# Performance work log

Measured on AMD Instinct MI355X. Metric: run time of the kernel, lower is better.

The kernel has to match this reference:

```python
import jax, jax.numpy as jnp
import numpy as np

B, T, E, H = 8, 1024, 512, 8  # batch, seq, emb (= per-head dim!), heads


def _layernorm(x, g, b, eps=1e-5):
    mu = jnp.mean(x, axis=-1, keepdims=True)
    var = jnp.var(x, axis=-1, keepdims=True)
    return (x - mu) * jax.lax.rsqrt(var + eps) * g + b


def setup_inputs() -> dict:
    key = jax.random.key(0)
    ks = jax.random.split(key, 8)
    s_in = 1.0 / np.sqrt(E)
    s_he = 1.0 / np.sqrt(H * E)
    return {
        "x": jax.random.normal(ks[0], (B, T, E), jnp.float32),
        "Wq": jax.random.normal(ks[1], (E, H * E), jnp.float32) * s_in,
        "bq": jnp.zeros((H * E,), jnp.float32),
        "Wk": jax.random.normal(ks[2], (E, H * E), jnp.float32) * s_in,
        "bk": jnp.zeros((H * E,), jnp.float32),
        "Wv": jax.random.normal(ks[3], (E, H * E), jnp.float32) * s_in,
        "bv": jnp.zeros((H * E,), jnp.float32),
        "Wu": jax.random.normal(ks[4], (H * E, E), jnp.float32) * s_he,
        "bu": jnp.zeros((E,), jnp.float32),
        "g1": jnp.ones((E,), jnp.float32),
        "b1": jnp.zeros((E,), jnp.float32),
        "Wh": jax.random.normal(ks[5], (E, E), jnp.float32) * s_in,
        "bh": jnp.zeros((E,), jnp.float32),
        "g2": jnp.ones((E,), jnp.float32),
        "b2": jnp.zeros((E,), jnp.float32),
    }


def reference(x, Wq, bq, Wk, bk, Wv, bv, Wu, bu, g1, b1, Wh, bh, g2, b2):
    b, t, e = x.shape
    h = Wq.shape[1] // e
    norm = 1.0 / np.sqrt(e)
    # projections: (b,t,h,e); each head gets full emb width per the source
    q = (x @ Wq + bq).reshape(b, t, h, e) * norm
    k = (x @ Wk + bk).reshape(b, t, h, e) * norm
    v = (x @ Wv + bv).reshape(b, t, h, e)
    # scores (b,h,t,t); Q and K are BOTH scaled (norm_factor applied to each)
    dot = jnp.einsum("bqhe,bkhe->bhqk", q, k)
    attn = jax.nn.softmax(dot, axis=-1)
    out = jnp.einsum("bhqk,bkhe->bqhe", attn, v)  # (b,t,h,e)
    out = out.reshape(b, t, h * e).sum(axis=1)     # sum over time -> (b,h*e)
    out = jax.nn.relu(out @ Wu + bu)               # unifyheads + active_func, (b,e)
    # dropout p=0 -> identity
    x = _layernorm(x + out[:, None, :], g1, b1)
    x = _layernorm(x + jax.nn.relu(x @ Wh + bh), g2, b2)
    return x
```

## Files before the change

kernel.cpp:

```cpp
#include <hip/hip_runtime.h>

#define BB 8
#define TT 1024
#define EE 512
#define HH 8
#define HEE 4096

typedef unsigned short u16;
typedef unsigned char u8;
typedef __bf16 bf16x8 __attribute__((ext_vector_type(8)));
typedef float floatx4 __attribute__((ext_vector_type(4)));
typedef float floatx2 __attribute__((ext_vector_type(2)));

__device__ __forceinline__ u16 f2bf(float f) {
    union { float f; unsigned int i; } v; v.f = f;
    unsigned int x = v.i;
    x += 0x7fffu + ((x >> 16) & 1u);
    return (u16)(x >> 16);
}
__device__ __forceinline__ float bf2f(u16 u) {
    union { unsigned int i; float f; } v; v.i = ((unsigned int)u) << 16; return v.f;
}
__device__ __forceinline__ void glds16(const u16* g, u16* l) {
    __builtin_amdgcn_global_load_lds(
        (const __attribute__((address_space(1))) void*)g,
        (__attribute__((address_space(3))) void*)l, 16, 0, 0);
}

__global__ __launch_bounds__(256) void convx_kernel(
    const float* __restrict__ x, u16* __restrict__ xb)
{
    size_t i = ((size_t)blockIdx.x * 256 + threadIdx.x) * 8;
    float4 a = *(const float4*)&x[i];
    float4 b = *(const float4*)&x[i + 4];
    union { u16 s[8]; uint4 v; } t;
    t.s[0] = f2bf(a.x); t.s[1] = f2bf(a.y); t.s[2] = f2bf(a.z); t.s[3] = f2bf(a.w);
    t.s[4] = f2bf(b.x); t.s[5] = f2bf(b.y); t.s[6] = f2bf(b.z); t.s[7] = f2bf(b.w);
    *(uint4*)&xb[i] = t.v;
}

__global__ __launch_bounds__(256) void transpose_wh(
    const float* __restrict__ Wh, u16* __restrict__ Wht)
{
    int n0 = blockIdx.x << 6, k0 = blockIdx.y << 6;
    __shared__ u16 tile[64][72];
    int tid = threadIdx.x;
    for (int rep = 0; rep < 4; rep++) {
        int lin = tid + (rep << 8);
        int r = lin >> 4, c4 = (lin & 15) << 2;
        float4 v = *(const float4*)&Wh[(size_t)(k0 + r) * EE + n0 + c4];
        union { u16 s[4]; uint2 u; } t;
        t.s[0] = f2bf(v.x); t.s[1] = f2bf(v.y); t.s[2] = f2bf(v.z); t.s[3] = f2bf(v.w);
        *(uint2*)&tile[r][c4] = t.u;
    }
    __syncthreads();
    for (int rep = 0; rep < 2; rep++) {
        int lin = tid + (rep << 8);
        int rr = lin >> 3, cc8 = (lin & 7) << 3;
        union { u16 s[8]; uint4 v; } tmp;
        #pragma unroll
        for (int u2 = 0; u2 < 8; u2++) tmp.s[u2] = tile[cc8 + u2][rr];
        *(uint4*)&Wht[(size_t)(n0 + rr) * EE + k0 + cc8] = tmp.v;
    }
}

__global__ __launch_bounds__(256) void mh_kernel(
    const float* __restrict__ Wq, const float* __restrict__ Wk, u16* __restrict__ Mt)
{
    __shared__ u16 As[128][40];
    __shared__ u16 Bs[128][40];
    int et = blockIdx.x, ft = blockIdx.y, h = blockIdx.z;
    int tid = threadIdx.x;
    int f0 = ft << 7, e0 = et << 7, hb = h << 9;
    int w = tid >> 6, lane = tid & 63;
    int g = lane >> 4, mn = lane & 15;
    int wm = (w >> 1) << 6, wn = (w & 1) << 6;
    floatx4 acc[4][4];
    floatx4 zero = {0.f, 0.f, 0.f, 0.f};
    for (int i = 0; i < 4; i++) for (int j = 0; j < 4; j++) acc[i][j] = zero;

    for (int kk = 0; kk < EE; kk += 32) {
        __syncthreads();
        for (int rep = 0; rep < 2; rep++) {
            int lin = tid + (rep << 8);
            int row = lin >> 2, c8 = (lin & 3) << 3;
            float4 va = *(const float4*)&Wk[(size_t)(f0 + row) * HEE + hb + kk + c8];
            float4 vb = *(const float4*)&Wk[(size_t)(f0 + row) * HEE + hb + kk + c8 + 4];
            union { u16 s[8]; uint4 v; } ta;
            ta.s[0]=f2bf(va.x); ta.s[1]=f2bf(va.y); ta.s[2]=f2bf(va.z); ta.s[3]=f2bf(va.w);
            ta.s[4]=f2bf(vb.x); ta.s[5]=f2bf(vb.y); ta.s[6]=f2bf(vb.z); ta.s[7]=f2bf(vb.w);
            *(uint4*)&As[row][c8] = ta.v;
            float4 vc = *(const float4*)&Wq[(size_t)(e0 + row) * HEE + hb + kk + c8];
            float4 vd = *(const float4*)&Wq[(size_t)(e0 + row) * HEE + hb + kk + c8 + 4];
            union { u16 s[8]; uint4 v; } tb;
            tb.s[0]=f2bf(vc.x); tb.s[1]=f2bf(vc.y); tb.s[2]=f2bf(vc.z); tb.s[3]=f2bf(vc.w);
            tb.s[4]=f2bf(vd.x); tb.s[5]=f2bf(vd.y); tb.s[6]=f2bf(vd.z); tb.s[7]=f2bf(vd.w);
            *(uint4*)&Bs[row][c8] = tb.v;
        }
        __syncthreads();
        bf16x8 af[4], bfr[4];
        #pragma unroll
        for (int i = 0; i < 4; i++) af[i]  = *(const bf16x8*)&As[wm + (i << 4) + mn][g << 3];
        #pragma unroll
        for (int j = 0; j < 4; j++) bfr[j] = *(const bf16x8*)&Bs[wn + (j << 4) + mn][g << 3];
        #pragma unroll
        for (int i = 0; i < 4; i++)
            #pragma unroll
            for (int j = 0; j < 4; j++)
                acc[i][j] = __builtin_amdgcn_mfma_f32_16x16x32_bf16(af[i], bfr[j], acc[i][j], 0, 0, 0);
    }
    const float norm2 = 0.001953125f;
    #pragma unroll
    for (int i = 0; i < 4; i++)
        #pragma unroll
        for (int j = 0; j < 4; j++) {
            int e = e0 + wn + (j << 4) + mn;
            #pragma unroll
            for (int r = 0; r < 4; r++) {
                int f = f0 + wm + (i << 4) + (g << 2) + r;
                Mt[(size_t)(hb + f) * EE + e] = f2bf(acc[i][j][r] * norm2);
            }
        }
}

__global__ __launch_bounds__(256) void p_proj(
    const u16* __restrict__ xb, const u16* __restrict__ Mt, u16* __restrict__ P)
{
    int id = blockIdx.x;
    int xcd = id & 7, v = id >> 3;
    int mt = v >> 2, cg = v & 3;
    int nt = (cg << 3) + xcd;
    __shared__ u16 As[128][32];
    __shared__ u16 Bs[128][32];
    int tid = threadIdx.x;
    int n0 = nt << 7, m0 = mt << 7;
    int w = tid >> 6, lane = tid & 63;
    int g = lane >> 4, mn = lane & 15;
    int wm = (w >> 1) << 6, wn = (w & 1) << 6;
    floatx4 acc[4][4];
    floatx4 zero = {0.f, 0.f, 0.f, 0.f};
    for (int i = 0; i < 4; i++) for (int j = 0; j < 4; j++) acc[i][j] = zero;

    int srow = tid >> 2, sc8 = (tid & 3) << 3;
    const u16* ga = xb + (size_t)(m0 + srow) * EE + sc8;
    const u16* gb = Mt + (size_t)(n0 + srow) * EE + sc8;
    u16* la = &As[0][0] + tid * 8;
    u16* lb = &Bs[0][0] + tid * 8;

    #pragma unroll
    for (int kk = 0; kk < EE; kk += 32) {
        __syncthreads();
        glds16(ga + kk, la);
        glds16(ga + kk + (size_t)64 * EE, la + 2048);
        glds16(gb + kk, lb);
        glds16(gb + kk + (size_t)64 * EE, lb + 2048);
        __syncthreads();
        bf16x8 af[4], bfr[4];
        #pragma unroll
        for (int i = 0; i < 4; i++) af[i]  = *(const bf16x8*)&As[wm + (i << 4) + mn][g << 3];
        #pragma unroll
        for (int j = 0; j < 4; j++) bfr[j] = *(const bf16x8*)&Bs[wn + (j << 4) + mn][g << 3];
        #pragma unroll
        for (int i = 0; i < 4; i++)
            #pragma unroll
            for (int j = 0; j < 4; j++)
                acc[i][j] = __builtin_amdgcn_mfma_f32_16x16x32_bf16(af[i], bfr[j], acc[i][j], 0, 0, 0);
    }
    #pragma unroll
    for (int i = 0; i < 4; i++)
        #pragma unroll
        for (int j = 0; j < 4; j++) {
            int col = n0 + wn + (j << 4) + mn;
            int h = col >> 9, f = col & 511;
            #pragma unroll
            for (int r = 0; r < 4; r++) {
                int row = m0 + wm + (i << 4) + (g << 2) + r;
                int bl = row >> 10, t = row & 1023;
                P[(((size_t)bl * HH + h) * TT + t) * EE + f] = f2bf(acc[i][j][r]);
            }
        }
}

__global__ __launch_bounds__(512) void spass1_kernel(
    const u16* __restrict__ P, const u16* __restrict__ xbf,
    u8* __restrict__ U, float* __restrict__ lpart)
{
    __shared__ u16 As[3][8192];
    __shared__ u16 Bs[3][8192];
    int id = blockIdx.x;
    int xcd = id & 7, v = id >> 3;
    int sl = ((v >> 4) << 3) + xcd;
    int tile = v & 15;
    int kt = tile >> 2, qt = tile & 3;
    int tid = threadIdx.x;
    int w = tid >> 6, lane = tid & 63;
    int g = lane >> 4, mn = lane & 15;
    int wm = w >> 2, wn = w & 3;

    const u16* Abase = xbf + ((size_t)(sl >> 3) * TT + (kt << 8)) * EE;
    const u16* Bbase = P   + ((size_t)sl * TT + (qt << 8)) * EE;

    int srow = tid >> 2;
    int cs = (tid & 3) ^ ((tid >> 3) & 3);
    const u16* gA = Abase + (size_t)srow * EE + (cs << 3);
    const u16* gB = Bbase + (size_t)srow * EE + (cs << 3);
    u16* lA = &As[0][0] + tid * 8;
    u16* lB = &Bs[0][0] + tid * 8;

    int coff = (g ^ ((mn >> 1) & 3)) << 3;
    int raBase = ((wm << 7) + mn) << 5;
    int rbBase = ((wn << 6) + mn) << 5;

    floatx4 acc[8][4];
    floatx4 zero = {0.f, 0.f, 0.f, 0.f};
    #pragma unroll
    for (int i = 0; i < 8; i++)
        #pragma unroll
        for (int j = 0; j < 4; j++) acc[i][j] = zero;

    #define STG_A(t, b) do { \
        glds16(gA + ((t) << 5),                    lA + (b) * 8192); \
        glds16(gA + ((t) << 5) + (size_t)128 * EE, lA + (b) * 8192 + 4096); \
    } while (0)
    #define STG_B(t, b) do { \
        glds16(gB + ((t) << 5),                    lB + (b) * 8192); \
        glds16(gB + ((t) << 5) + (size_t)128 * EE, lB + (b) * 8192 + 4096); \
    } while (0)

    STG_A(0, 0); STG_B(0, 0);
    STG_A(1, 1); STG_B(1, 1);
    asm volatile("s_waitcnt vmcnt(4)" ::: "memory");
    __builtin_amdgcn_s_barrier();
    __builtin_amdgcn_sched_barrier(0);

    #pragma unroll
    for (int t = 0; t < 16; t++) {
        const int cur = t % 3;
        const int nxt = (t + 2) % 3;
        bf16x8 af0[4], bfr[4];
        #pragma unroll
        for (int i = 0; i < 4; i++)
            af0[i] = *(const bf16x8*)&As[cur][raBase + (i << 9) + coff];
        #pragma unroll
        for (int j = 0; j < 4; j++)
            bfr[j] = *(const bf16x8*)&Bs[cur][rbBase + (j << 9) + coff];
        if (t < 14) STG_A(t + 2, nxt);
        __builtin_amdgcn_sched_barrier(0);
        __builtin_amdgcn_s_barrier();
        asm volatile("s_waitcnt lgkmcnt(0)" ::: "memory");
        __builtin_amdgcn_sched_barrier(0);
        __builtin_amdgcn_s_setprio(1);
        #pragma unroll
        for (int i = 0; i < 4; i++)
            #pragma unroll
            for (int j = 0; j < 4; j++)
                acc[i][j] = __builtin_amdgcn_mfma_f32_16x16x32_bf16(af0[i], bfr[j], acc[i][j], 0, 0, 0);
        __builtin_amdgcn_s_setprio(0);
        __builtin_amdgcn_sched_barrier(0);
        __builtin_amdgcn_s_barrier();
        bf16x8 af1[4];
        #pragma unroll
        for (int i = 0; i < 4; i++)
            af1[i] = *(const bf16x8*)&As[cur][raBase + ((i + 4) << 9) + coff];
        if (t < 14) STG_B(t + 2, nxt);
        __builtin_amdgcn_sched_barrier(0);
        __builtin_amdgcn_s_barrier();
        asm volatile("s_waitcnt lgkmcnt(0)" ::: "memory");
        __builtin_amdgcn_sched_barrier(0);
        __builtin_amdgcn_s_setprio(1);
        #pragma unroll
        for (int i = 0; i < 4; i++)
            #pragma unroll
            for (int j = 0; j < 4; j++)
                acc[i + 4][j] = __builtin_amdgcn_mfma_f32_16x16x32_bf16(af1[i], bfr[j], acc[i + 4][j], 0, 0, 0);
        __builtin_amdgcn_s_setprio(0);
        __builtin_amdgcn_sched_barrier(0);
        if (t < 14)      asm volatile("s_waitcnt vmcnt(4)" ::: "memory");
        else if (t == 14) asm volatile("s_waitcnt vmcnt(0)" ::: "memory");
        __builtin_amdgcn_s_barrier();
        __builtin_amdgcn_sched_barrier(0);
    }
    #undef STG_A
    #undef STG_B

    float rsj[4] = {0.f, 0.f, 0.f, 0.f};
    u8* Ub = U + ((size_t)sl << 20) + (kt << 8) + (wm << 7) + (g << 2);
    #pragma unroll
    for (int j = 0; j < 4; j++) {
        int q = (qt << 8) + (wn << 6) + (j << 4) + mn;
        u8* Uq = Ub + ((size_t)q << 10);
        #pragma unroll
        for (int i = 0; i < 8; i++) {
            float e0 = __expf(acc[i][j][0]);
            float e1 = __expf(acc[i][j][1]);
            float e2 = __expf(acc[i][j][2]);
            float e3 = __expf(acc[i][j][3]);
            rsj[j] += (e0 + e1) + (e2 + e3);
            int pk = __builtin_amdgcn_cvt_pk_fp8_f32(e0, e1, 0, false);
            pk = __builtin_amdgcn_cvt_pk_fp8_f32(e2, e3, pk, true);
            *(unsigned int*)(Uq + (i << 4)) = (unsigned int)pk;
        }
    }
    #pragma unroll
    for (int j = 0; j < 4; j++) {
        rsj[j] += __shfl_xor(rsj[j], 16, 64);
        rsj[j] += __shfl_xor(rsj[j], 32, 64);
    }
    float* red = (float*)&As[0][0];
    if (g == 0) {
        #pragma unroll
        for (int j = 0; j < 4; j++)
            red[(wm << 8) + (wn << 6) + (j << 4) + mn] = rsj[j];
    }
    __syncthreads();
    if (tid < 256) {
        float s = red[tid] + red[256 + tid];
        lpart[(((size_t)(sl * 4 + kt)) << 10) + (qt << 8) + tid] = s;
    }
}

__global__ __launch_bounds__(256) void colreduce_kernel(
    const u8* __restrict__ U, const float* __restrict__ lpart,
    float* __restrict__ wpart)
{
    __shared__ float lin[128];
    int sl = blockIdx.x, qc = blockIdx.y;
    int tid = threadIdx.x;
    if (tid < 128) {
        float s = 0.f;
        #pragma unroll
        for (int kt = 0; kt < 4; kt++)
            s += lpart[((size_t)(sl * 4 + kt) << 10) + (qc << 7) + tid];
        lin[tid] = 1.f / s;
    }
    __syncthreads();
    const u8* Us = U + ((size_t)sl << 20) + ((size_t)(qc << 7) << 10) + (tid << 2);
    float a0 = 0.f, a1 = 0.f, a2 = 0.f, a3 = 0.f;
    #pragma unroll 8
    for (int q = 0; q < 128; q++) {
        unsigned int d = *(const unsigned int*)(Us + ((size_t)q << 10));
        float l = lin[q];
        floatx2 lo = __builtin_amdgcn_cvt_pk_f32_fp8((int)d, false);
        floatx2 hi = __builtin_amdgcn_cvt_pk_f32_fp8((int)d, true);
        a0 += l * lo[0];
        a1 += l * lo[1];
        a2 += l * hi[0];
        a3 += l * hi[1];
    }
    float4 res = {a0, a1, a2, a3};
    *(float4*)&wpart[(((size_t)sl * 8 + qc) << 10) + (tid << 2)] = res;
}

__global__ __launch_bounds__(256) void sv_kernel(
    const u16* __restrict__ xb, const float* __restrict__ wpart, float* __restrict__ sVp)
{
    __shared__ float wl[8][128];
    int b = blockIdx.x, kq = blockIdx.y;
    int tid = threadIdx.x;
    #pragma unroll
    for (int rep = 0; rep < 4; rep++) {
        int idx = tid + (rep << 8);
        int h = idx >> 7, k = idx & 127;
        float s = 0.f;
        #pragma unroll
        for (int qt = 0; qt < 8; qt++)
            s += wpart[(((size_t)(b * 8 + h)) * 8 + qt) * TT + (kq << 7) + k];
        wl[h][k] = s;
    }
    __syncthreads();
    const u16* xr = xb + ((size_t)b * TT + (kq << 7)) * EE;
    float a0[8], a1[8];
    #pragma unroll
    for (int h = 0; h < 8; h++) { a0[h] = 0.f; a1[h] = 0.f; }
    for (int k = 0; k < 128; k++) {
        float x0 = bf2f(xr[(size_t)k * EE + tid]);
        float x1 = bf2f(xr[(size_t)k * EE + tid + 256]);
        #pragma unroll
        for (int h = 0; h < 8; h++) {
            float wk = wl[h][k];
            a0[h] += wk * x0;
            a1[h] += wk * x1;
        }
    }
    #pragma unroll
    for (int h = 0; h < 8; h++) {
        sVp[((size_t)b * 8 + kq) * HEE + (h << 9) + tid]       = a0[h];
        sVp[((size_t)b * 8 + kq) * HEE + (h << 9) + tid + 256] = a1[h];
    }
}

__global__ __launch_bounds__(256) void out1_kernel(
    const float* __restrict__ sVp, const float* __restrict__ Wv,
    const float* __restrict__ bv, float* __restrict__ o1)
{
    __shared__ float s[8][512];
    __shared__ float part[4][8][64];
    int h = blockIdx.x, ec = blockIdx.y;
    int tid = threadIdx.x;
    for (int idx = tid; idx < 8 * 512; idx += 256) {
        int b = idx >> 9, e = idx & 511;
        float acc = 0.f;
        #pragma unroll
        for (int kq = 0; kq < 8; kq++)
            acc += sVp[((size_t)b * 8 + kq) * HEE + (h << 9) + e];
        s[b][e] = acc;
    }
    __syncthreads();
    int cl = tid & 63, eq = tid >> 6;
    int col = (h << 9) + (ec << 6) + cl;
    float a[8];
    #pragma unroll
    for (int b = 0; b < 8; b++) a[b] = 0.f;
    for (int e = eq << 7; e < (eq << 7) + 128; e++) {
        float wv = Wv[(size_t)e * HEE + col];
        #pragma unroll
        for (int b = 0; b < 8; b++) a[b] += s[b][e] * wv;
    }
    #pragma unroll
    for (int b = 0; b < 8; b++) part[eq][b][cl] = a[b];
    __syncthreads();
    #pragma unroll
    for (int r = 0; r < 2; r++) {
        int idx2 = tid + (r << 8);
        int b = idx2 >> 6, c2 = idx2 & 63;
        int col2 = (h << 9) + (ec << 6) + c2;
        float vv = part[0][b][c2] + part[1][b][c2] + part[2][b][c2] + part[3][b][c2]
                 + 1024.f * bv[col2];
        o1[(size_t)b * HEE + col2] = vv;
    }
}

__global__ __launch_bounds__(256) void out2_kernel(
    const float* __restrict__ o1, const float* __restrict__ Wu, float* __restrict__ o2p)
{
    __shared__ float o1s[8][128];
    __shared__ float part[4][8][64];
    int jc = blockIdx.x, ec = blockIdx.y;
    int tid = threadIdx.x;
    #pragma unroll
    for (int it = 0; it < 4; it++) {
        int idx = tid + (it << 8);
        int b = idx >> 7, jj = idx & 127;
        o1s[b][jj] = o1[(size_t)b * HEE + (jc << 7) + jj];
    }
    __syncthreads();
    int el = tid & 63, jq = tid >> 6;
    int col = (ec << 6) + el;
    const float* wu = Wu + (size_t)((jc << 7) + (jq << 5)) * EE + col;
    float a[8];
    #pragma unroll
    for (int b = 0; b < 8; b++) a[b] = 0.f;
    #pragma unroll 4
    for (int jj = 0; jj < 32; jj++) {
        float wv = wu[(size_t)jj * EE];
        int j = (jq << 5) + jj;
        #pragma unroll
        for (int b = 0; b < 8; b++) a[b] += o1s[b][j] * wv;
    }
    #pragma unroll
    for (int b = 0; b < 8; b++) part[jq][b][el] = a[b];
    __syncthreads();
    #pragma unroll
    for (int it = 0; it < 2; it++) {
        int idx = tid + (it << 8);
        int b = idx >> 6, e2 = idx & 63;
        float vv = part[0][b][e2] + part[1][b][e2] + part[2][b][e2] + part[3][b][e2];
        o2p[((size_t)b * 32 + jc) * EE + (ec << 6) + e2] = vv;
    }
}

__global__ __launch_bounds__(512) void out2_reduce(
    const float* __restrict__ o2p, const float* __restrict__ bu, float* __restrict__ o2)
{
    int b = blockIdx.x, tid = threadIdx.x;
    float s = bu[tid];
    for (int jc = 0; jc < 32; jc++)
        s += o2p[((size_t)b * 32 + jc) * EE + tid];
    o2[(size_t)b * EE + tid] = fmaxf(s, 0.f);
}

__global__ __launch_bounds__(256) void tail_fused(
    const float* __restrict__ x, const float* __restrict__ o2,
    const float* __restrict__ g1, const float* __restrict__ b1,
    const u16* __restrict__ Wht, const float* __restrict__ bh,
    const float* __restrict__ g2, const float* __restrict__ b2,
    float* __restrict__ out)
{
    __shared__ u16 Ys[32][520];
    __shared__ u16 Bs[512][32];
    __shared__ float redS[4][32];
    __shared__ float redQ[4][32];
    int tid = threadIdx.x;
    int m0 = blockIdx.x << 5;
    int b = m0 >> 10;
    int w = tid >> 6, lane = tid & 63;
    int g = lane >> 4, mn = lane & 15;

    {
        int c8 = lane << 3;
        float ob[8], g1v[8], b1v[8];
        ((float4*)ob)[0]  = *(const float4*)&o2[(size_t)b * EE + c8];
        ((float4*)ob)[1]  = *(const float4*)&o2[(size_t)b * EE + c8 + 4];
        ((float4*)g1v)[0] = *(const float4*)&g1[c8];
        ((float4*)g1v)[1] = *(const float4*)&g1[c8 + 4];
        ((float4*)b1v)[0] = *(const float4*)&b1[c8];
        ((float4*)b1v)[1] = *(const float4*)&b1[c8 + 4];
        for (int iter = 0; iter < 8; iter++) {
            int row = w + (iter << 2);
            const float* xr = x + (size_t)(m0 + row) * EE + c8;
            float v[8];
            ((float4*)v)[0] = *(const float4*)&xr[0];
            ((float4*)v)[1] = *(const float4*)&xr[4];
            float s = 0.f, q = 0.f;
            #pragma unroll
            for (int u2 = 0; u2 < 8; u2++) {
                v[u2] += ob[u2];
                s += v[u2];
                q += v[u2] * v[u2];
            }
            #pragma unroll
            for (int off = 1; off < 64; off <<= 1) {
                s += __shfl_xor(s, off, 64);
                q += __shfl_xor(q, off, 64);
            }
            float mean = s * (1.f / EE);
            float var = q * (1.f / EE) - mean * mean;
            float rstd = rsqrtf(var + 1e-5f);
            union { u16 us[8]; uint4 uv; } pk;
            #pragma unroll
            for (int u2 = 0; u2 < 8; u2++)
                pk.us[u2] = f2bf((v[u2] - mean) * rstd * g1v[u2] + b1v[u2]);
            *(uint4*)&Ys[row][c8] = pk.uv;
        }
    }

    int n0w = w << 7;
    floatx4 acc[2][8];
    floatx4 zero = {0.f, 0.f, 0.f, 0.f};
    for (int i = 0; i < 2; i++) for (int j = 0; j < 8; j++) acc[i][j] = zero;

    for (int kk = 0; kk < EE; kk += 32) {
        __syncthreads();
        #pragma unroll
        for (int c = 0; c < 8; c++) {
            int lin = (c << 8) + tid;
            int nrow = lin >> 2, k8 = (lin & 3) << 3;
            glds16(Wht + (size_t)nrow * EE + kk + k8, &Bs[0][0] + lin * 8);
        }
        __syncthreads();
        bf16x8 af[2], bfr[8];
        #pragma unroll
        for (int i = 0; i < 2; i++)
            af[i] = *(const bf16x8*)&Ys[(i << 4) + mn][kk + (g << 3)];
        #pragma unroll
        for (int j = 0; j < 8; j++)
            bfr[j] = *(const bf16x8*)&Bs[n0w + (j << 4) + mn][g << 3];
        #pragma unroll
        for (int i = 0; i < 2; i++)
            #pragma unroll
            for (int j = 0; j < 8; j++)
                acc[i][j] = __builtin_amdgcn_mfma_f32_16x16x32_bf16(af[i], bfr[j], acc[i][j], 0, 0, 0);
    }

    float bh8[8], g28[8], b28[8];
    #pragma unroll
    for (int j = 0; j < 8; j++) {
        int col = n0w + (j << 4) + mn;
        bh8[j] = bh[col]; g28[j] = g2[col]; b28[j] = b2[col];
    }
    float ps[2][4], pq[2][4];
    #pragma unroll
    for (int i = 0; i < 2; i++)
        #pragma unroll
        for (int r = 0; r < 4; r++) { ps[i][r] = 0.f; pq[i][r] = 0.f; }
    #pragma unroll
    for (int i = 0; i < 2; i++)
        #pragma unroll
        for (int j = 0; j < 8; j++) {
            int col = n0w + (j << 4) + mn;
            #pragma unroll
            for (int r = 0; r < 4; r++) {
                int row = (i << 4) + (g << 2) + r;
                float zv = fmaxf(acc[i][j][r] + bh8[j], 0.f) + bf2f(Ys[row][col]);
                acc[i][j][r] = zv;
                ps[i][r] += zv;
                pq[i][r] += zv * zv;
            }
        }
    #pragma unroll
    for (int off = 1; off < 16; off <<= 1) {
        #pragma unroll
        for (int i = 0; i < 2; i++)
            #pragma unroll
            for (int r = 0; r < 4; r++) {
                ps[i][r] += __shfl_xor(ps[i][r], off, 64);
                pq[i][r] += __shfl_xor(pq[i][r], off, 64);
            }
    }
    if (mn == 0) {
        #pragma unroll
        for (int i = 0; i < 2; i++)
            #pragma unroll
            for (int r = 0; r < 4; r++) {
                int row = (i << 4) + (g << 2) + r;
                redS[w][row] = ps[i][r];
                redQ[w][row] = pq[i][r];
            }
    }
    __syncthreads();
    #pragma unroll
    for (int i = 0; i < 2; i++)
        #pragma unroll
        for (int r = 0; r < 4; r++) {
            int row = (i << 4) + (g << 2) + r;
            float s = redS[0][row] + redS[1][row] + redS[2][row] + redS[3][row];
            float q = redQ[0][row] + redQ[1][row] + redQ[2][row] + redQ[3][row];
            float mean = s * (1.f / EE);
            float var = q * (1.f / EE) - mean * mean;
            float rstd = rsqrtf(var + 1e-5f);
            #pragma unroll
            for (int j = 0; j < 8; j++) {
                int col = n0w + (j << 4) + mn;
                out[(size_t)(m0 + row) * EE + col] =
                    (acc[i][j][r] - mean) * rstd * g28[j] + b28[j];
            }
        }
}

extern "C" void kernel_launch(void* const* d_in, const int* in_sizes, int n_in,
                              void* d_out, int out_size, void* d_ws, size_t ws_size,
                              hipStream_t stream)
{
    const float* x  = (const float*)d_in[0];
    const float* Wq = (const float*)d_in[1];
    const float* Wk = (const float*)d_in[3];
    const float* Wv = (const float*)d_in[5];
    const float* bv = (const float*)d_in[6];
    const float* Wu = (const float*)d_in[7];
    const float* bu = (const float*)d_in[8];
    const float* g1 = (const float*)d_in[9];
    const float* b1 = (const float*)d_in[10];
    const float* Wh = (const float*)d_in[11];
    const float* bh = (const float*)d_in[12];
    const float* g2 = (const float*)d_in[13];
    const float* b2 = (const float*)d_in[14];
    float* out = (float*)d_out;

    char* p = (char*)d_ws;
    u16* Wht = (u16*)p;    p += (size_t)EE * EE * 2;
    u16* xbf = (u16*)p;    p += (size_t)BB * TT * EE * 2;
    u16* Mt  = (u16*)p;    p += (size_t)HEE * EE * 2;
    float* lpart = (float*)p; p += (size_t)64 * 8 * TT * 4;
    float* wpart = (float*)p; p += (size_t)64 * 8 * TT * 4;
    float* sVp   = (float*)p; p += (size_t)BB * 8 * HEE * 4;
    float* o1    = (float*)p; p += (size_t)BB * HEE * 4;
    float* o2p   = (float*)p; p += (size_t)BB * 32 * EE * 4;
    float* o2    = (float*)p; p += (size_t)BB * EE * 4;
    u16* P  = (u16*)p;     p += (size_t)BB * HH * TT * EE * 2;
    u8* U   = (u8*)p;      p += (size_t)64 * TT * TT;

    convx_kernel<<<dim3(2048), 256, 0, stream>>>(x, xbf);
    transpose_wh<<<dim3(8, 8), 256, 0, stream>>>(Wh, Wht);
    mh_kernel<<<dim3(4, 4, 8), 256, 0, stream>>>(Wq, Wk, Mt);
    p_proj<<<dim3(2048), 256, 0, stream>>>(xbf, Mt, P);
    spass1_kernel<<<dim3(1024), 512, 0, stream>>>(P, xbf, U, lpart);
    colreduce_kernel<<<dim3(64, 8), 256, 0, stream>>>(U, lpart, wpart);
    sv_kernel<<<dim3(8, 8), 256, 0, stream>>>(xbf, wpart, sVp);
    out1_kernel<<<dim3(8, 8), 256, 0, stream>>>(sVp, Wv, bv, o1);
    out2_kernel<<<dim3(32, 8), 256, 0, stream>>>(o1, Wu, o2p);
    out2_reduce<<<dim3(8), 512, 0, stream>>>(o2p, bu, o2);
    tail_fused<<<dim3(256), 256, 0, stream>>>(x, o2, g1, b1, Wht, bh, g2, b2, out);
}
```

Before: 355.8 us.

## Fuse P projection into score kernel, merge prep kernels, atomic out2 reduction

The P = x·M projection is now computed per (batch, head, 128-query tile) inside the score kernel and kept in shared memory, so the large bf16 P tensor is never written to or read back from global memory. Inside the same block it then loops over four key tiles to compute exp scores, writes fp8 U through a shared-memory staging buffer, and emits the row-sum partials. The x conversion, the Wh transpose and the o2 bias init are merged into one launch. out2 now accumulates with atomicAdd into o2, with the ReLU moved into tail_fused, which removes the separate reduce kernel. In exchange the fused kernel uses large shared memory (160KB) and launches only 512 blocks, which limits occupancy. Float atomics also make the summation order nondeterministic.

```diff
diff --git a/kernel.cpp b/kernel.cpp
--- a/kernel.cpp
+++ b/kernel.cpp
@@ -27,40 +27,46 @@
         (__attribute__((address_space(3))) void*)l, 16, 0, 0);
 }
 
-__global__ __launch_bounds__(256) void convx_kernel(
-    const float* __restrict__ x, u16* __restrict__ xb)
-{
-    size_t i = ((size_t)blockIdx.x * 256 + threadIdx.x) * 8;
-    float4 a = *(const float4*)&x[i];
-    float4 b = *(const float4*)&x[i + 4];
-    union { u16 s[8]; uint4 v; } t;
-    t.s[0] = f2bf(a.x); t.s[1] = f2bf(a.y); t.s[2] = f2bf(a.z); t.s[3] = f2bf(a.w);
-    t.s[4] = f2bf(b.x); t.s[5] = f2bf(b.y); t.s[6] = f2bf(b.z); t.s[7] = f2bf(b.w);
-    *(uint4*)&xb[i] = t.v;
-}
-
-__global__ __launch_bounds__(256) void transpose_wh(
-    const float* __restrict__ Wh, u16* __restrict__ Wht)
-{
-    int n0 = blockIdx.x << 6, k0 = blockIdx.y << 6;
+__global__ __launch_bounds__(256) void prep_kernel(
+    const float* __restrict__ x, u16* __restrict__ xb,
+    const float* __restrict__ Wh, u16* __restrict__ Wht,
+    const float* __restrict__ bu, float* __restrict__ o2)
+{
     __shared__ u16 tile[64][72];
-    int tid = threadIdx.x;
-    for (int rep = 0; rep < 4; rep++) {
-        int lin = tid + (rep << 8);
-        int r = lin >> 4, c4 = (lin & 15) << 2;
-        float4 v = *(const float4*)&Wh[(size_t)(k0 + r) * EE + n0 + c4];
-        union { u16 s[4]; uint2 u; } t;
-        t.s[0] = f2bf(v.x); t.s[1] = f2bf(v.y); t.s[2] = f2bf(v.z); t.s[3] = f2bf(v.w);
-        *(uint2*)&tile[r][c4] = t.u;
-    }
-    __syncthreads();
-    for (int rep = 0; rep < 2; rep++) {
-        int lin = tid + (rep << 8);
-        int rr = lin >> 3, cc8 = (lin & 7) << 3;
-        union { u16 s[8]; uint4 v; } tmp;
-        #pragma unroll
-        for (int u2 = 0; u2 < 8; u2++) tmp.s[u2] = tile[cc8 + u2][rr];
-        *(uint4*)&Wht[(size_t)(n0 + rr) * EE + k0 + cc8] = tmp.v;
+    int bid = blockIdx.x;
+    int tid = threadIdx.x;
+    if (bid < 2048) {
+        size_t i = ((size_t)bid * 256 + tid) * 8;
+        float4 a = *(const float4*)&x[i];
+        float4 b = *(const float4*)&x[i + 4];
+        union { u16 s[8]; uint4 v; } t;
+        t.s[0] = f2bf(a.x); t.s[1] = f2bf(a.y); t.s[2] = f2bf(a.z); t.s[3] = f2bf(a.w);
+        t.s[4] = f2bf(b.x); t.s[5] = f2bf(b.y); t.s[6] = f2bf(b.z); t.s[7] = f2bf(b.w);
+        *(uint4*)&xb[i] = t.v;
+    } else if (bid < 2112) {
+        int tb = bid - 2048;
+        int n0 = (tb & 7) << 6, k0 = (tb >> 3) << 6;
+        for (int rep = 0; rep < 4; rep++) {
+            int lin = tid + (rep << 8);
+            int r = lin >> 4, c4 = (lin & 15) << 2;
+            float4 v = *(const float4*)&Wh[(size_t)(k0 + r) * EE + n0 + c4];
+            union { u16 s[4]; uint2 u; } t;
+            t.s[0] = f2bf(v.x); t.s[1] = f2bf(v.y); t.s[2] = f2bf(v.z); t.s[3] = f2bf(v.w);
+            *(uint2*)&tile[r][c4] = t.u;
+        }
+        __syncthreads();
+        for (int rep = 0; rep < 2; rep++) {
+            int lin = tid + (rep << 8);
+            int rr = lin >> 3, cc8 = (lin & 7) << 3;
+            union { u16 s[8]; uint4 v; } tmp;
+            #pragma unroll
+            for (int u2 = 0; u2 < 8; u2++) tmp.s[u2] = tile[cc8 + u2][rr];
+            *(uint4*)&Wht[(size_t)(n0 + rr) * EE + k0 + cc8] = tmp.v;
+        }
+    } else {
+        int r = bid - 2112;
+        int b = r >> 1, half = (r & 1) << 8;
+        o2[(size_t)b * EE + half + tid] = bu[half + tid];
     }
 }
 
@@ -123,93 +129,30 @@
         }
 }
 
-__global__ __launch_bounds__(256) void p_proj(
-    const u16* __restrict__ xb, const u16* __restrict__ Mt, u16* __restrict__ P)
-{
+__global__ __launch_bounds__(512) void pqs_kernel(
+    const u16* __restrict__ xbf, const u16* __restrict__ Mt,
+    u8* __restrict__ U, float* __restrict__ lpart)
+{
+    __shared__ __align__(16) u8 SMEM[163840];
+    u16* SM = (u16*)SMEM;
     int id = blockIdx.x;
     int xcd = id & 7, v = id >> 3;
-    int mt = v >> 2, cg = v & 3;
-    int nt = (cg << 3) + xcd;
-    __shared__ u16 As[128][32];
-    __shared__ u16 Bs[128][32];
-    int tid = threadIdx.x;
-    int n0 = nt << 7, m0 = mt << 7;
+    int b = xcd;
+    int h = v >> 3;
+    int qt = v & 7;
+    int sl = (b << 3) + h;
+    int tid = threadIdx.x;
     int w = tid >> 6, lane = tid & 63;
     int g = lane >> 4, mn = lane & 15;
-    int wm = (w >> 1) << 6, wn = (w & 1) << 6;
-    floatx4 acc[4][4];
-    floatx4 zero = {0.f, 0.f, 0.f, 0.f};
-    for (int i = 0; i < 4; i++) for (int j = 0; j < 4; j++) acc[i][j] = zero;
-
-    int srow = tid >> 2, sc8 = (tid & 3) << 3;
-    const u16* ga = xb + (size_t)(m0 + srow) * EE + sc8;
-    const u16* gb = Mt + (size_t)(n0 + srow) * EE + sc8;
-    u16* la = &As[0][0] + tid * 8;
-    u16* lb = &Bs[0][0] + tid * 8;
-
-    #pragma unroll
-    for (int kk = 0; kk < EE; kk += 32) {
-        __syncthreads();
-        glds16(ga + kk, la);
-        glds16(ga + kk + (size_t)64 * EE, la + 2048);
-        glds16(gb + kk, lb);
-        glds16(gb + kk + (size_t)64 * EE, lb + 2048);
-        __syncthreads();
-        bf16x8 af[4], bfr[4];
-        #pragma unroll
-        for (int i = 0; i < 4; i++) af[i]  = *(const bf16x8*)&As[wm + (i << 4) + mn][g << 3];
-        #pragma unroll
-        for (int j = 0; j < 4; j++) bfr[j] = *(const bf16x8*)&Bs[wn + (j << 4) + mn][g << 3];
-        #pragma unroll
-        for (int i = 0; i < 4; i++)
-            #pragma unroll
-            for (int j = 0; j < 4; j++)
-                acc[i][j] = __builtin_amdgcn_mfma_f32_16x16x32_bf16(af[i], bfr[j], acc[i][j], 0, 0, 0);
-    }
-    #pragma unroll
-    for (int i = 0; i < 4; i++)
-        #pragma unroll
-        for (int j = 0; j < 4; j++) {
-            int col = n0 + wn + (j << 4) + mn;
-            int h = col >> 9, f = col & 511;
-            #pragma unroll
-            for (int r = 0; r < 4; r++) {
-                int row = m0 + wm + (i << 4) + (g << 2) + r;
-                int bl = row >> 10, t = row & 1023;
-                P[(((size_t)bl * HH + h) * TT + t) * EE + f] = f2bf(acc[i][j][r]);
-            }
-        }
-}
-
-__global__ __launch_bounds__(512) void spass1_kernel(
-    const u16* __restrict__ P, const u16* __restrict__ xbf,
-    u8* __restrict__ U, float* __restrict__ lpart)
-{
-    __shared__ u16 As[3][8192];
-    __shared__ u16 Bs[3][8192];
-    int id = blockIdx.x;
-    int xcd = id & 7, v = id >> 3;
-    int sl = ((v >> 4) << 3) + xcd;
-    int tile = v & 15;
-    int kt = tile >> 2, qt = tile & 3;
-    int tid = threadIdx.x;
-    int w = tid >> 6, lane = tid & 63;
-    int g = lane >> 4, mn = lane & 15;
-    int wm = w >> 2, wn = w & 3;
-
-    const u16* Abase = xbf + ((size_t)(sl >> 3) * TT + (kt << 8)) * EE;
-    const u16* Bbase = P   + ((size_t)sl * TT + (qt << 8)) * EE;
 
     int srow = tid >> 2;
     int cs = (tid & 3) ^ ((tid >> 3) & 3);
-    const u16* gA = Abase + (size_t)srow * EE + (cs << 3);
-    const u16* gB = Bbase + (size_t)srow * EE + (cs << 3);
-    u16* lA = &As[0][0] + tid * 8;
-    u16* lB = &Bs[0][0] + tid * 8;
-
     int coff = (g ^ ((mn >> 1) & 3)) << 3;
-    int raBase = ((wm << 7) + mn) << 5;
-    int rbBase = ((wn << 6) + mn) << 5;
+
+    const u16* gA1 = xbf + (size_t)((b << 10) + (qt << 7) + srow) * EE + (cs << 3);
+    const u16* gB1 = Mt  + (size_t)((h << 9) + srow) * EE + (cs << 3);
+    u16* lA1 = SM + tid * 8;
+    u16* lB1 = SM + 12288 + tid * 8;
 
     floatx4 acc[8][4];
     floatx4 zero = {0.f, 0.f, 0.f, 0.f};
@@ -218,18 +161,17 @@
         #pragma unroll
         for (int j = 0; j < 4; j++) acc[i][j] = zero;
 
-    #define STG_A(t, b) do { \
-        glds16(gA + ((t) << 5),                    lA + (b) * 8192); \
-        glds16(gA + ((t) << 5) + (size_t)128 * EE, lA + (b) * 8192 + 4096); \
+    #define STG1(t, bf) do { \
+        glds16(gA1 + ((t) << 5),          lA1 + (bf) * 4096); \
+        glds16(gB1 + ((t) << 5),          lB1 + (bf) * 16384); \
+        glds16(gB1 + ((t) << 5) + 65536,  lB1 + (bf) * 16384 + 4096); \
+        glds16(gB1 + ((t) << 5) + 131072, lB1 + (bf) * 16384 + 8192); \
+        glds16(gB1 + ((t) << 5) + 196608, lB1 + (bf) * 16384 + 12288); \
     } while (0)
-    #define STG_B(t, b) do { \
-        glds16(gB + ((t) << 5),                    lB + (b) * 8192); \
-        glds16(gB + ((t) << 5) + (size_t)128 * EE, lB + (b) * 8192 + 4096); \
-    } while (0)
-
-    STG_A(0, 0); STG_B(0, 0);
-    STG_A(1, 1); STG_B(1, 1);
-    asm volatile("s_waitcnt vmcnt(4)" ::: "memory");
+
+    STG1(0, 0);
+    STG1(1, 1);
+    asm volatile("s_waitcnt vmcnt(5)" ::: "memory");
     __builtin_amdgcn_s_barrier();
     __builtin_amdgcn_sched_barrier(0);
 
@@ -237,86 +179,157 @@
     for (int t = 0; t < 16; t++) {
         const int cur = t % 3;
         const int nxt = (t + 2) % 3;
-        bf16x8 af0[4], bfr[4];
-        #pragma unroll
-        for (int i = 0; i < 4; i++)
-            af0[i] = *(const bf16x8*)&As[cur][raBase + (i << 9) + coff];
+        bf16x8 af[8], bfr[4];
+        #pragma unroll
+        for (int i = 0; i < 8; i++)
+            af[i] = *(const bf16x8*)&SM[cur * 4096 + (((i << 4) + mn) << 5) + coff];
         #pragma unroll
         for (int j = 0; j < 4; j++)
-            bfr[j] = *(const bf16x8*)&Bs[cur][rbBase + (j << 9) + coff];
-        if (t < 14) STG_A(t + 2, nxt);
+            bfr[j] = *(const bf16x8*)&SM[12288 + cur * 16384 + ((w >> 1) << 12)
+                                         + ((((w & 1) << 6) + (j << 4) + mn) << 5) + coff];
+        if (t < 14) STG1(t + 2, nxt);
         __builtin_amdgcn_sched_barrier(0);
         __builtin_amdgcn_s_barrier();
         asm volatile("s_waitcnt lgkmcnt(0)" ::: "memory");
         __builtin_amdgcn_sched_barrier(0);
         __builtin_amdgcn_s_setprio(1);
         #pragma unroll
-        for (int i = 0; i < 4; i++)
+        for (int i = 0; i < 8; i++)
             #pragma unroll
             for (int j = 0; j < 4; j++)
-                acc[i][j] = __builtin_amdgcn_mfma_f32_16x16x32_bf16(af0[i], bfr[j], acc[i][j], 0, 0, 0);
+                acc[i][j] = __builtin_amdgcn_mfma_f32_16x16x32_bf16(af[i], bfr[j], acc[i][j], 0, 0, 0);
         __builtin_amdgcn_s_setprio(0);
         __builtin_amdgcn_sched_barrier(0);
-        __builtin_amdgcn_s_barrier();
-        bf16x8 af1[4];
-        #pragma unroll
-        for (int i = 0; i < 4; i++)
-            af1[i] = *(const bf16x8*)&As[cur][raBase + ((i + 4) << 9) + coff];
-        if (t < 14) STG_B(t + 2, nxt);
-        __builtin_amdgcn_sched_barrier(0);
-        __builtin_amdgcn_s_barrier();
-        asm volatile("s_waitcnt lgkmcnt(0)" ::: "memory");
-        __builtin_amdgcn_sched_barrier(0);
-        __builtin_amdgcn_s_setprio(1);
-        #pragma unroll
-        for (int i = 0; i < 4; i++)
-            #pragma unroll
-            for (int j = 0; j < 4; j++)
-                acc[i + 4][j] = __builtin_amdgcn_mfma_f32_16x16x32_bf16(af1[i], bfr[j], acc[i + 4][j], 0, 0, 0);
-        __builtin_amdgcn_s_setprio(0);
-        __builtin_amdgcn_sched_barrier(0);
-        if (t < 14)      asm volatile("s_waitcnt vmcnt(4)" ::: "memory");
+        if (t < 14)       asm volatile("s_waitcnt vmcnt(5)" ::: "memory");
         else if (t == 14) asm volatile("s_waitcnt vmcnt(0)" ::: "memory");
         __builtin_amdgcn_s_barrier();
         __builtin_amdgcn_sched_barrier(0);
     }
-    #undef STG_A
-    #undef STG_B
-
-    float rsj[4] = {0.f, 0.f, 0.f, 0.f};
-    u8* Ub = U + ((size_t)sl << 20) + (kt << 8) + (wm << 7) + (g << 2);
-    #pragma unroll
-    for (int j = 0; j < 4; j++) {
-        int q = (qt << 8) + (wn << 6) + (j << 4) + mn;
-        u8* Uq = Ub + ((size_t)q << 10);
+    #undef STG1
+
+    {
+        u16* Pl = SM + 16384;
         #pragma unroll
         for (int i = 0; i < 8; i++) {
-            float e0 = __expf(acc[i][j][0]);
-            float e1 = __expf(acc[i][j][1]);
-            float e2 = __expf(acc[i][j][2]);
-            float e3 = __expf(acc[i][j][3]);
-            rsj[j] += (e0 + e1) + (e2 + e3);
-            int pk = __builtin_amdgcn_cvt_pk_fp8_f32(e0, e1, 0, false);
-            pk = __builtin_amdgcn_cvt_pk_fp8_f32(e2, e3, pk, true);
-            *(unsigned int*)(Uq + (i << 4)) = (unsigned int)pk;
-        }
-    }
-    #pragma unroll
-    for (int j = 0; j < 4; j++) {
-        rsj[j] += __shfl_xor(rsj[j], 16, 64);
-        rsj[j] += __shfl_xor(rsj[j], 32, 64);
-    }
-    float* red = (float*)&As[0][0];
-    if (g == 0) {
-        #pragma unroll
-        for (int j = 0; j < 4; j++)
-            red[(wm << 8) + (wn << 6) + (j << 4) + mn] = rsj[j];
-    }
-    __syncthreads();
-    if (tid < 256) {
-        float s = red[tid] + red[256 + tid];
-        lpart[(((size_t)(sl * 4 + kt)) << 10) + (qt << 8) + tid] = s;
-    }
+            #pragma unroll
+            for (int r = 0; r < 4; r++) {
+                int q = (i << 4) + (g << 2) + r;
+                int sw = (q >> 1) & 3;
+                #pragma unroll
+                for (int j = 0; j < 4; j++) {
+                    int f = (w << 6) + (j << 4) + mn;
+                    Pl[(q << 9) + (((f >> 3) ^ sw) << 3) + (f & 7)] = f2bf(acc[i][j][r]);
+                }
+            }
+        }
+    }
+    __syncthreads();
+
+    const u16* gA2 = xbf + (size_t)((b << 10) + srow) * EE + (cs << 3);
+    u16* lA2 = SM + tid * 8;
+    int wm2 = w >> 1, wn2 = w & 1;
+    int msw = (mn >> 1) & 3;
+
+    #define STG2(kt, t, bf) do { \
+        glds16(gA2 + (size_t)((kt) << 8) * EE + ((t) << 5),           lA2 + (bf) * 8192); \
+        glds16(gA2 + (size_t)(((kt) << 8) + 128) * EE + ((t) << 5),   lA2 + (bf) * 8192 + 4096); \
+    } while (0)
+
+    for (int kt = 0; kt < 4; kt++) {
+        floatx4 acc2[4][4];
+        #pragma unroll
+        for (int i = 0; i < 4; i++)
+            #pragma unroll
+            for (int j = 0; j < 4; j++) acc2[i][j] = zero;
+
+        __syncthreads();
+        STG2(kt, 0, 0);
+        asm volatile("s_waitcnt vmcnt(0)" ::: "memory");
+        __syncthreads();
+
+        #pragma unroll
+        for (int t = 0; t < 16; t++) {
+            const int cur = t & 1;
+            bf16x8 af2[4], bfr2[4];
+            #pragma unroll
+            for (int i = 0; i < 4; i++)
+                af2[i] = *(const bf16x8*)&SM[cur * 8192 + ((wm2 >> 1) << 12)
+                                             + ((((wm2 & 1) << 6) + (i << 4) + mn) << 5) + coff];
+            #pragma unroll
+            for (int j = 0; j < 4; j++) {
+                int q = (wn2 << 6) + (j << 4) + mn;
+                bfr2[j] = *(const bf16x8*)&SM[16384 + (q << 9)
+                                              + ((((t << 2) + g) ^ msw) << 3)];
+            }
+            if (t < 15) STG2(kt, t + 1, cur ^ 1);
+            __builtin_amdgcn_sched_barrier(0);
+            __builtin_amdgcn_s_barrier();
+            asm volatile("s_waitcnt lgkmcnt(0)" ::: "memory");
+            __builtin_amdgcn_sched_barrier(0);
+            __builtin_amdgcn_s_setprio(1);
+            #pragma unroll
+            for (int i = 0; i < 4; i++)
+                #pragma unroll
+                for (int j = 0; j < 4; j++)
+                    acc2[i][j] = __builtin_amdgcn_mfma_f32_16x16x32_bf16(af2[i], bfr2[j], acc2[i][j], 0, 0, 0);
+            __builtin_amdgcn_s_setprio(0);
+            __builtin_amdgcn_sched_barrier(0);
+            if (t < 15) asm volatile("s_waitcnt vmcnt(0)" ::: "memory");
+            __builtin_amdgcn_s_barrier();
+            __builtin_amdgcn_sched_barrier(0);
+        }
+
+        float rsj[4] = {0.f, 0.f, 0.f, 0.f};
+        u8* Ut = SMEM;
+        #pragma unroll
+        for (int p = 0; p < 2; p++) {
+            __syncthreads();
+            if (wn2 == p) {
+                #pragma unroll
+                for (int j = 0; j < 4; j++) {
+                    int qloc = (j << 4) + mn;
+                    u8* Urow = Ut + qloc * 272 + (wm2 << 6) + (g << 2);
+                    #pragma unroll
+                    for (int i = 0; i < 4; i++) {
+                        float e0 = __expf(acc2[i][j][0]);
+                        float e1 = __expf(acc2[i][j][1]);
+                        float e2 = __expf(acc2[i][j][2]);
+                        float e3 = __expf(acc2[i][j][3]);
+                        rsj[j] += (e0 + e1) + (e2 + e3);
+                        int pk = __builtin_amdgcn_cvt_pk_fp8_f32(e0, e1, 0, false);
+                        pk = __builtin_amdgcn_cvt_pk_fp8_f32(e2, e3, pk, true);
+                        *(unsigned int*)(Urow + (i << 4)) = (unsigned int)pk;
+                    }
+                }
+            }
+            __syncthreads();
+            u8* Ub = U + ((size_t)sl << 20) + ((size_t)((qt << 7) + (p << 6)) << 10) + (kt << 8);
+            #pragma unroll
+            for (int it = 0; it < 8; it++) {
+                int ql = (it << 3) + w;
+                unsigned int vv = *(const unsigned int*)(Ut + ql * 272 + (lane << 2));
+                *(unsigned int*)(Ub + ((size_t)ql << 10) + (lane << 2)) = vv;
+            }
+        }
+        #pragma unroll
+        for (int j = 0; j < 4; j++) {
+            rsj[j] += __shfl_xor(rsj[j], 16, 64);
+            rsj[j] += __shfl_xor(rsj[j], 32, 64);
+        }
+        float* red = (float*)(SMEM + 24576);
+        __syncthreads();
+        if (g == 0) {
+            #pragma unroll
+            for (int j = 0; j < 4; j++)
+                red[(wm2 << 7) + (wn2 << 6) + (j << 4) + mn] = rsj[j];
+        }
+        __syncthreads();
+        if (tid < 128) {
+            float s = red[tid] + red[128 + tid] + red[256 + tid] + red[384 + tid];
+            lpart[(((size_t)(sl * 4 + kt)) << 10) + (qt << 7) + tid] = s;
+        }
+    }
+    #undef STG2
 }
 
 __global__ __launch_bounds__(256) void colreduce_kernel(
@@ -431,7 +444,7 @@
 }
 
 __global__ __launch_bounds__(256) void out2_kernel(
-    const float* __restrict__ o1, const float* __restrict__ Wu, float* __restrict__ o2p)
+    const float* __restrict__ o1, const float* __restrict__ Wu, float* __restrict__ o2)
 {
     __shared__ float o1s[8][128];
     __shared__ float part[4][8][64];
@@ -465,18 +478,8 @@
         int idx = tid + (it << 8);
         int b = idx >> 6, e2 = idx & 63;
         float vv = part[0][b][e2] + part[1][b][e2] + part[2][b][e2] + part[3][b][e2];
-        o2p[((size_t)b * 32 + jc) * EE + (ec << 6) + e2] = vv;
-    }
-}
-
-__global__ __launch_bounds__(512) void out2_reduce(
-    const float* __restrict__ o2p, const float* __restrict__ bu, float* __restrict__ o2)
-{
-    int b = blockIdx.x, tid = threadIdx.x;
-    float s = bu[tid];
-    for (int jc = 0; jc < 32; jc++)
-        s += o2p[((size_t)b * 32 + jc) * EE + tid];
-    o2[(size_t)b * EE + tid] = fmaxf(s, 0.f);
+        atomicAdd(&o2[(size_t)b * EE + (ec << 6) + e2], vv);
+    }
 }
 
 __global__ __launch_bounds__(256) void tail_fused(
@@ -501,6 +504,8 @@
         float ob[8], g1v[8], b1v[8];
         ((float4*)ob)[0]  = *(const float4*)&o2[(size_t)b * EE + c8];
         ((float4*)ob)[1]  = *(const float4*)&o2[(size_t)b * EE + c8 + 4];
+        #pragma unroll
+        for (int u2 = 0; u2 < 8; u2++) ob[u2] = fmaxf(ob[u2], 0.f);
         ((float4*)g1v)[0] = *(const float4*)&g1[c8];
         ((float4*)g1v)[1] = *(const float4*)&g1[c8 + 4];
         ((float4*)b1v)[0] = *(const float4*)&b1[c8];
@@ -654,20 +659,15 @@
     float* wpart = (float*)p; p += (size_t)64 * 8 * TT * 4;
     float* sVp   = (float*)p; p += (size_t)BB * 8 * HEE * 4;
     float* o1    = (float*)p; p += (size_t)BB * HEE * 4;
-    float* o2p   = (float*)p; p += (size_t)BB * 32 * EE * 4;
     float* o2    = (float*)p; p += (size_t)BB * EE * 4;
-    u16* P  = (u16*)p;     p += (size_t)BB * HH * TT * EE * 2;
     u8* U   = (u8*)p;      p += (size_t)64 * TT * TT;
 
-    convx_kernel<<<dim3(2048), 256, 0, stream>>>(x, xbf);
-    transpose_wh<<<dim3(8, 8), 256, 0, stream>>>(Wh, Wht);
+    prep_kernel<<<dim3(2128), 256, 0, stream>>>(x, xbf, Wh, Wht, bu, o2);
     mh_kernel<<<dim3(4, 4, 8), 256, 0, stream>>>(Wq, Wk, Mt);
-    p_proj<<<dim3(2048), 256, 0, stream>>>(xbf, Mt, P);
-    spass1_kernel<<<dim3(1024), 512, 0, stream>>>(P, xbf, U, lpart);
+    pqs_kernel<<<dim3(512), 512, 0, stream>>>(xbf, Mt, U, lpart);
     colreduce_kernel<<<dim3(64, 8), 256, 0, stream>>>(U, lpart, wpart);
     sv_kernel<<<dim3(8, 8), 256, 0, stream>>>(xbf, wpart, sVp);
     out1_kernel<<<dim3(8, 8), 256, 0, stream>>>(sVp, Wv, bv, o1);
-    out2_kernel<<<dim3(32, 8), 256, 0, stream>>>(o1, Wu, o2p);
-    out2_reduce<<<dim3(8), 512, 0, stream>>>(o2p, bu, o2);
+    out2_kernel<<<dim3(32, 8), 256, 0, stream>>>(o1, Wu, o2);
     tail_fused<<<dim3(256), 256, 0, stream>>>(x, o2, g1, b1, Wht, bh, g2, b2, out);
 }
```

New measurement: 326.4 us. 8.3% less time.
